# Kernel tuning notes

Measured on AMD Instinct MI355X. Metric: run time of the kernel, lower is better.

Reference implementation:

```python
import jax, jax.numpy as jnp
import numpy as np
from jax.scipy.special import logsumexp

E = 512      # input_size (= 2*hidden_size)
T = 24       # output_size (num CRF tags)
B, S = 32, 512
HEADS = 2


def setup_inputs() -> dict:
    key = jax.random.key(0)
    ks = jax.random.split(key, 12)
    u = lambda k, shape, a: jax.random.uniform(k, shape, jnp.float32, -a, a)
    inp = {
        "encoder_outputs": jax.random.normal(ks[0], (B, S, E), jnp.float32),
        "labels": jax.random.randint(ks[1], (B, S), 0, T),
        "mask": jnp.ones((B, S), dtype=bool),
        # nn.MultiheadAttention params
        "Win": u(ks[2], (3 * E, E), E ** -0.5),
        "bin_": jnp.zeros((3 * E,), jnp.float32),
        "Wout": u(ks[3], (E, E), E ** -0.5),
        "bout": jnp.zeros((E,), jnp.float32),
        # crf_linear
        "crf_w": u(ks[4], (T, E), E ** -0.5),
        "crf_b": u(ks[5], (T,), E ** -0.5),
        # torchcrf CRF params (uniform(-0.1, 0.1))
        "start_t": u(ks[6], (T,), 0.1),
        "end_t": u(ks[7], (T,), 0.1),
        "trans": u(ks[8], (T, T), 0.1),
        # entity_linear
        "ent_w": u(ks[9], (2, E), E ** -0.5),
        "ent_b": u(ks[10], (2,), E ** -0.5),
    }
    return inp


def _mha(x, Win, bin_, Wout, bout):
    b, s, e = x.shape
    hd = e // HEADS
    qkv = x @ Win.T + bin_                       # [B,S,3E]
    q, k, v = jnp.split(qkv, 3, axis=-1)
    q = q.reshape(b, s, HEADS, hd)
    k = k.reshape(b, s, HEADS, hd)
    v = v.reshape(b, s, HEADS, hd)
    scores = jnp.einsum("bqhd,bkhd->bhqk", q, k) / jnp.sqrt(jnp.float32(hd))
    attn = jax.nn.softmax(scores, axis=-1)       # [B,H,S,S]
    out = jnp.einsum("bhqk,bkhd->bqhd", attn, v).reshape(b, s, e)
    return out @ Wout.T + bout


def _crf_numerator(em, labels, maskf, start_t, end_t, trans):
    # em: [B,S,T] emissions, labels: [B,S] int, maskf: [B,S] float (mask[:,0]==1)
    bidx = jnp.arange(em.shape[0])
    score = start_t[labels[:, 0]] + em[bidx, 0, labels[:, 0]]
    prev, cur = labels[:, :-1], labels[:, 1:]
    em_t = jnp.take_along_axis(em[:, 1:], cur[:, :, None], axis=2)[..., 0]
    score = score + ((trans[prev, cur] + em_t) * maskf[:, 1:]).sum(axis=1)
    seq_ends = maskf.sum(axis=1).astype(jnp.int32) - 1
    last_tags = labels[bidx, seq_ends]
    return score + end_t[last_tags]


def _crf_normalizer(em, maskf, start_t, end_t, trans):
    score0 = start_t + em[:, 0]                  # [B,T]

    def step(score, x):
        e_t, m_t = x                             # [B,T], [B]
        nxt = logsumexp(score[:, :, None] + trans[None] + e_t[:, None, :], axis=1)
        return jnp.where(m_t[:, None] > 0, nxt, score), None

    xs = (em[:, 1:].swapaxes(0, 1), maskf[:, 1:].T)
    score, _ = jax.lax.scan(step, score0, xs)
    return logsumexp(score + end_t, axis=1)


def _viterbi(em, start_t, end_t, trans):
    # decode is called without a mask -> mask of all ones
    score0 = start_t + em[:, 0]                  # [B,T]

    def step(score, e_t):
        nxt = score[:, :, None] + trans[None] + e_t[:, None, :]  # [B,T,T]
        return nxt.max(axis=1), nxt.argmax(axis=1)

    score, history = jax.lax.scan(step, score0, em[:, 1:].swapaxes(0, 1))
    last = jnp.argmax(score + end_t, axis=1)     # [B]

    def back(tag, hist):
        prev = jnp.take_along_axis(hist, tag[:, None], axis=1)[:, 0]
        return prev, prev

    _, prevs = jax.lax.scan(back, last, history, reverse=True)  # [S-1,B]
    return jnp.concatenate([prevs, last[None]], axis=0).T       # [B,S]


def reference(encoder_outputs, labels, mask, Win, bin_, Wout, bout,
              crf_w, crf_b, start_t, end_t, trans, ent_w, ent_b):
    attn = _mha(encoder_outputs, Win, bin_, Wout, bout)
    dec = jax.nn.relu(attn)                      # [B,S,E]
    fc_out = dec @ crf_w.T + crf_b               # [B,S,T]
    maskf = mask.astype(fc_out.dtype)
    num = _crf_numerator(fc_out, labels, maskf, start_t, end_t, trans)
    den = _crf_normalizer(fc_out, maskf, start_t, end_t, trans)
    llh = (num - den).sum() / maskf.sum()        # reduction='token_mean'
    crf_out = _viterbi(fc_out, start_t, end_t, trans)
    seg_out = jax.nn.log_softmax(dec @ ent_w.T + ent_b, axis=2)
    return crf_out, seg_out, -llh
```

## Files before the change

### kernel.cpp

```cpp
#include <hip/hip_runtime.h>

#define BB 32
#define SS 512
#define EE 512
#define NHH 2
#define HDD 256
#define E3 1536
#define NT 24
#define MR (BB*SS)

typedef _Float16 half8  __attribute__((ext_vector_type(8)));
typedef _Float16 half4v __attribute__((ext_vector_type(4)));
typedef float    f32x4  __attribute__((ext_vector_type(4)));

__device__ __forceinline__ float rl(float v, int l) {
    return __int_as_float(__builtin_amdgcn_readlane(__float_as_int(v), l));
}

template<int BN>
__global__ __launch_bounds__(256) void mfma_gemm(
    const float* __restrict__ A, int lda, long sAhi, long sAlo, int zA,
    const float* __restrict__ B, int ldb, long sBhi, long sBlo, int zB,
    const float* __restrict__ bias,
    float* __restrict__ C, int ldc, long sChi, long sClo, int zC,
    int K, int relu)
{
    __shared__ __align__(16) _Float16 sAh[8*640];
    __shared__ __align__(16) _Float16 sAl[8*640];
    __shared__ __align__(16) _Float16 sBh[8*640];
    __shared__ __align__(16) _Float16 sBl[8*640];

    const int t = threadIdx.x;
    const int z = blockIdx.z;
    const int za = zA + z, zb = zB + z, zc = zC + z;
    const float* Ab = A + (size_t)(za>>1)*sAhi + (size_t)(za&1)*sAlo
                        + (size_t)blockIdx.y*128*lda;
    const float* Bb = B + (size_t)(zb>>1)*sBhi + (size_t)(zb&1)*sBlo
                        + (BN ? (size_t)blockIdx.x*128
                              : (size_t)blockIdx.x*128*ldb);

    const int wv = t >> 6, lane = t & 63;
    const int wm = wv >> 1, wn = wv & 1;
    const int lm = lane & 15, lq = lane >> 4;

    f32x4 acc[4][4];
#pragma unroll
    for (int i = 0; i < 4; ++i)
#pragma unroll
        for (int j = 0; j < 4; ++j) acc[i][j] = (f32x4){0.f,0.f,0.f,0.f};

    const int r8  = t >> 3;
    const int kc  = (t & 7) * 4;
    const int bnk = (t >> 7) * 16;
    const int bnn = t & 127;

    for (int k0 = 0; k0 < K; k0 += 32) {
        float4 ga[4], gb[4]; float gv[16];
#pragma unroll
        for (int i = 0; i < 4; ++i)
            ga[i] = *(const float4*)(Ab + (size_t)(r8 + 32*i)*lda + k0 + kc);
        if (BN) {
#pragma unroll
            for (int i = 0; i < 16; ++i)
                gv[i] = Bb[(size_t)(k0 + bnk + i)*ldb + bnn];
        } else {
#pragma unroll
            for (int i = 0; i < 4; ++i)
                gb[i] = *(const float4*)(Bb + (size_t)(r8 + 32*i)*ldb + k0 + kc);
        }
        __syncthreads();
#pragma unroll
        for (int i = 0; i < 4; ++i) {
            const int row  = r8 + 32*i;
            const int base = (row >> 4)*640 + (row & 15)*40 + kc;
            float4 a = ga[i];
            _Float16 h0 = (_Float16)a.x, h1 = (_Float16)a.y,
                     h2 = (_Float16)a.z, h3 = (_Float16)a.w;
            _Float16 l0 = (_Float16)(a.x - (float)h0),
                     l1 = (_Float16)(a.y - (float)h1),
                     l2 = (_Float16)(a.z - (float)h2),
                     l3 = (_Float16)(a.w - (float)h3);
            *(half4v*)&sAh[base] = (half4v){h0,h1,h2,h3};
            *(half4v*)&sAl[base] = (half4v){l0,l1,l2,l3};
        }
        if (BN) {
#pragma unroll
            for (int i = 0; i < 16; ++i) {
                const int k = bnk + i;
                float v = gv[i];
                _Float16 h = (_Float16)v;
                _Float16 l = (_Float16)(v - (float)h);
                const int base = (bnn >> 4)*640 + (bnn & 15)*40 + k;
                sBh[base] = h;
                sBl[base] = l;
            }
        } else {
#pragma unroll
            for (int i = 0; i < 4; ++i) {
                const int row  = r8 + 32*i;
                const int base = (row >> 4)*640 + (row & 15)*40 + kc;
                float4 b = gb[i];
                _Float16 h0 = (_Float16)b.x, h1 = (_Float16)b.y,
                         h2 = (_Float16)b.z, h3 = (_Float16)b.w;
                _Float16 l0 = (_Float16)(b.x - (float)h0),
                         l1 = (_Float16)(b.y - (float)h1),
                         l2 = (_Float16)(b.z - (float)h2),
                         l3 = (_Float16)(b.w - (float)h3);
                *(half4v*)&sBh[base] = (half4v){h0,h1,h2,h3};
                *(half4v*)&sBl[base] = (half4v){l0,l1,l2,l3};
            }
        }
        __syncthreads();

        half8 bhf[4], blf[4];
#pragma unroll
        for (int j = 0; j < 4; ++j) {
            const int tb = (wn*4 + j)*640 + lm*40 + lq*8;
            bhf[j] = *(const half8*)&sBh[tb];
            blf[j] = *(const half8*)&sBl[tb];
        }
#pragma unroll
        for (int i = 0; i < 4; ++i) {
            const int ta = (wm*4 + i)*640 + lm*40 + lq*8;
            half8 ah = *(const half8*)&sAh[ta];
            half8 al = *(const half8*)&sAl[ta];
#pragma unroll
            for (int j = 0; j < 4; ++j) {
                acc[i][j] = __builtin_amdgcn_mfma_f32_16x16x32_f16(ah, bhf[j], acc[i][j], 0, 0, 0);
                acc[i][j] = __builtin_amdgcn_mfma_f32_16x16x32_f16(al, bhf[j], acc[i][j], 0, 0, 0);
                acc[i][j] = __builtin_amdgcn_mfma_f32_16x16x32_f16(ah, blf[j], acc[i][j], 0, 0, 0);
            }
        }
    }

    float* Cb = C + (size_t)(zc>>1)*sChi + (size_t)(zc&1)*sClo;
#pragma unroll
    for (int j = 0; j < 4; ++j) {
        const int col = blockIdx.x*128 + (wn*4 + j)*16 + lm;
        const float bj = bias ? bias[col] : 0.f;
#pragma unroll
        for (int i = 0; i < 4; ++i) {
            const int row0 = blockIdx.y*128 + (wm*4 + i)*16 + lq*4;
#pragma unroll
            for (int r = 0; r < 4; ++r) {
                float v = acc[i][j][r] + bj;
                if (relu) v = fmaxf(v, 0.f);
                Cb[(size_t)(row0 + r)*ldc + col] = v;
            }
        }
    }
}

__global__ __launch_bounds__(256) void softmax_rows(float* __restrict__ scores)
{
    const int w    = threadIdx.x >> 6;
    const int lane = threadIdx.x & 63;
    const size_t row = (size_t)blockIdx.x * 4 + w;
    float* p = scores + row * SS + lane * 8;
    float4 v0 = *(float4*)(p);
    float4 v1 = *(float4*)(p + 4);
    const float scale = 0.0625f;
    float m = fmaxf(fmaxf(fmaxf(v0.x, v0.y), fmaxf(v0.z, v0.w)),
                    fmaxf(fmaxf(v1.x, v1.y), fmaxf(v1.z, v1.w)));
#pragma unroll
    for (int off = 32; off >= 1; off >>= 1) m = fmaxf(m, __shfl_xor(m, off));
    v0.x = __expf((v0.x - m) * scale); v0.y = __expf((v0.y - m) * scale);
    v0.z = __expf((v0.z - m) * scale); v0.w = __expf((v0.w - m) * scale);
    v1.x = __expf((v1.x - m) * scale); v1.y = __expf((v1.y - m) * scale);
    v1.z = __expf((v1.z - m) * scale); v1.w = __expf((v1.w - m) * scale);
    float sum = v0.x + v0.y + v0.z + v0.w + v1.x + v1.y + v1.z + v1.w;
#pragma unroll
    for (int off = 32; off >= 1; off >>= 1) sum += __shfl_xor(sum, off);
    float inv = 1.f / sum;
    v0.x *= inv; v0.y *= inv; v0.z *= inv; v0.w *= inv;
    v1.x *= inv; v1.y *= inv; v1.z *= inv; v1.w *= inv;
    *(float4*)(p)     = v0;
    *(float4*)(p + 4) = v1;
}

__global__ __launch_bounds__(192) void fc_crf_kernel(
    const float* __restrict__ dec, const float* __restrict__ W,
    const float* __restrict__ bias, float* __restrict__ out)
{
    __shared__ __align__(16) float Ws[NT][516];
    for (int i = threadIdx.x; i < NT*128; i += 192) {
        int j = i >> 7, c = (i & 127) * 4;
        *(float4*)&Ws[j][c] = *(const float4*)(W + (size_t)j*EE + c);
    }
    __syncthreads();
    const int t = threadIdx.x;
    const int rloc = t / NT;
    const int j = t - rloc * NT;
    const int row = blockIdx.x * 8 + rloc;
    const float4* a = (const float4*)(dec + (size_t)row * EE);
    float acc = 0.f;
#pragma unroll 4
    for (int i = 0; i < 128; ++i) {
        float4 x = a[i];
        float4 y = *(const float4*)&Ws[j][i*4];
        acc += x.x*y.x + x.y*y.y + x.z*y.z + x.w*y.w;
    }
    out[(size_t)row * NT + j] = acc + bias[j];
}

__global__ __launch_bounds__(64, 1) void crf_seg_kernel(
    const float* __restrict__ fc, const int* __restrict__ labels,
    const float* __restrict__ start_t, const float* __restrict__ end_t,
    const float* __restrict__ trans, const float* __restrict__ dec,
    const float* __restrict__ ent_w, const float* __restrict__ ent_b,
    float* __restrict__ num, float* __restrict__ den,
    float* __restrict__ crf_out, float* __restrict__ segout)
{
    __shared__ __align__(16) float fc_lds[SS*NT];
    __shared__ unsigned char hist[(SS-1)*NT];

    const int blk  = blockIdx.x;
    const int lane = threadIdx.x;

    if (blk >= 96) {
        const int row = blk - 96;
        const float4* a  = (const float4*)(dec + (size_t)row * EE);
        const float4* w0 = (const float4*)(ent_w);
        const float4* w1 = (const float4*)(ent_w + EE);
        float acc0 = 0.f, acc1 = 0.f;
#pragma unroll
        for (int i = 0; i < 2; ++i) {
            int idx = lane * 2 + i;
            float4 x = a[idx];
            float4 u = w0[idx];
            float4 v = w1[idx];
            acc0 += x.x*u.x + x.y*u.y + x.z*u.z + x.w*u.w;
            acc1 += x.x*v.x + x.y*v.y + x.z*v.z + x.w*v.w;
        }
#pragma unroll
        for (int off = 32; off >= 1; off >>= 1) {
            acc0 += __shfl_xor(acc0, off);
            acc1 += __shfl_xor(acc1, off);
        }
        if (lane == 0) {
            float l0 = acc0 + ent_b[0];
            float l1 = acc1 + ent_b[1];
            float m  = fmaxf(l0, l1);
            float lse = m + __logf(__expf(l0 - m) + __expf(l1 - m));
            segout[(size_t)row*2 + 0] = l0 - lse;
            segout[(size_t)row*2 + 1] = l1 - lse;
        }
        return;
    }

    const int role = blk >> 5;
    const int b    = blk & 31;
    const float* fcb = fc + (size_t)b * SS * NT;

    if (role == 2) {
        float acc = 0.f;
        for (int s = 1 + lane; s < SS; s += 64) {
            int prev = labels[b*SS + s - 1];
            int cur  = labels[b*SS + s];
            acc += trans[prev*NT + cur] + fcb[(size_t)s*NT + cur];
        }
        if (lane == 0) {
            int l0 = labels[b*SS];
            acc += start_t[l0] + fcb[l0] + end_t[labels[b*SS + SS - 1]];
        }
#pragma unroll
        for (int off = 32; off >= 1; off >>= 1) acc += __shfl_xor(acc, off);
        if (lane == 0) num[b] = acc;
        return;
    }

#pragma unroll
    for (int i = 0; i < SS*NT/256; ++i) {
        const int idx = i*256 + lane*4;
        *(float4*)&fc_lds[idx] = *(const float4*)(fcb + idx);
    }
    __syncthreads();

    const int j = (lane < NT) ? lane : 0;
    float sc = start_t[j] + fc_lds[j];

    if (role == 0) {
        float etr[NT];
#pragma unroll
        for (int i = 0; i < NT; ++i) etr[i] = __expf(trans[i*NT + j]);
        float em_next = fc_lds[NT + j];
        for (int s = 1; s < SS; ++s) {
            float em = em_next;
            int snx = (s + 1 < SS) ? s + 1 : s;
            em_next = fc_lds[snx * NT + j];
            const float m  = __builtin_amdgcn_readfirstlane(sc);
            const float eo = __expf(sc - m);
            float a0 = 0.f, a1 = 0.f, a2 = 0.f, a3 = 0.f;
#pragma unroll
            for (int i = 0; i < NT; i += 4) {
                a0 = fmaf(rl(eo, i+0), etr[i+0], a0);
                a1 = fmaf(rl(eo, i+1), etr[i+1], a1);
                a2 = fmaf(rl(eo, i+2), etr[i+2], a2);
                a3 = fmaf(rl(eo, i+3), etr[i+3], a3);
            }
            sc = m + __logf((a0 + a1) + (a2 + a3)) + em;
        }
        float v = (lane < NT) ? sc + end_t[j] : -1e30f;
        float m2 = v;
#pragma unroll
        for (int off = 32; off >= 1; off >>= 1) m2 = fmaxf(m2, __shfl_xor(m2, off));
        float e = (lane < NT) ? __expf(v - m2) : 0.f;
#pragma unroll
        for (int off = 32; off >= 1; off >>= 1) e += __shfl_xor(e, off);
        if (lane == 0) den[b] = m2 + __logf(e);
    } else {
        float trC[NT];
#pragma unroll
        for (int i = 0; i < NT; ++i) trC[i] = trans[i*NT + j];
        float em_next = fc_lds[NT + j];
        for (int s = 1; s < SS; ++s) {
            float em = em_next;
            int snx = (s + 1 < SS) ? s + 1 : s;
            em_next = fc_lds[snx * NT + j];
            float tv[NT]; int ti[NT];
#pragma unroll
            for (int i = 0; i < NT; ++i) { tv[i] = rl(sc, i) + trC[i]; ti[i] = i; }
#pragma unroll
            for (int st = 1; st < NT; st <<= 1)
#pragma unroll
                for (int i = 0; i + st < NT; i += 2*st)
                    if (tv[i+st] > tv[i]) { tv[i] = tv[i+st]; ti[i] = ti[i+st]; }
            sc = tv[0] + em;
            if (lane < NT) hist[(s-1)*NT + lane] = (unsigned char)ti[0];
        }
        float bv = (lane < NT) ? sc + end_t[j] : -1e30f;
        int bi = (lane < NT) ? lane : NT;
#pragma unroll
        for (int off = 32; off >= 1; off >>= 1) {
            float ov = __shfl_xor(bv, off);
            int   oi = __shfl_xor(bi, off);
            if (ov > bv || (ov == bv && oi < bi)) { bv = ov; bi = oi; }
        }
        __syncthreads();
        if (lane == 0) {
            int tag = bi;
            crf_out[(size_t)b*SS + SS - 1] = (float)tag;
            for (int s = SS - 2; s >= 0; --s) {
                tag = hist[s*NT + tag];
                crf_out[(size_t)b*SS + s] = (float)tag;
            }
        }
    }
}

__global__ __launch_bounds__(64) void llh_kernel(
    const float* __restrict__ num, const float* __restrict__ den,
    float* __restrict__ out)
{
    int t = threadIdx.x;
    float v = (t < BB) ? (num[t] - den[t]) : 0.f;
#pragma unroll
    for (int off = 32; off >= 1; off >>= 1) v += __shfl_xor(v, off);
    if (t == 0) out[(size_t)MR * 3] = -(v / (float)MR);
}

extern "C" void kernel_launch(void* const* d_in, const int* in_sizes, int n_in,
                              void* d_out, int out_size, void* d_ws, size_t ws_size,
                              hipStream_t stream) {
    const float* enc     = (const float*)d_in[0];
    const int*   labels  = (const int*)  d_in[1];
    const float* Win     = (const float*)d_in[3];
    const float* bin     = (const float*)d_in[4];
    const float* Wout    = (const float*)d_in[5];
    const float* bout    = (const float*)d_in[6];
    const float* crf_w   = (const float*)d_in[7];
    const float* crf_b   = (const float*)d_in[8];
    const float* start_t = (const float*)d_in[9];
    const float* end_t   = (const float*)d_in[10];
    const float* trans   = (const float*)d_in[11];
    const float* ent_w   = (const float*)d_in[12];
    const float* ent_b   = (const float*)d_in[13];
    float* out = (float*)d_out;

    float* ws   = (float*)d_ws;
    float* qkv  = ws;
    float* attn = qkv  + (size_t)MR * E3;
    float* big  = attn + (size_t)MR * EE;
    float* sch  = big;
    float* dec  = big;
    float* fc   = big  + (size_t)MR * EE;
    float* num  = fc   + (size_t)MR * NT;
    float* den  = num  + BB;

    dim3 blk(256);
    mfma_gemm<0><<<dim3(E3/128, MR/128, 1), blk, 0, stream>>>(
        enc, EE, 0, 0, 0,  Win, EE, 0, 0, 0,  bin,
        qkv, E3, 0, 0, 0,  EE, 0);
    for (int p = 0; p < 2; ++p) {
        int zoff = p * 32;
        mfma_gemm<0><<<dim3(SS/128, SS/128, 32), blk, 0, stream>>>(
            qkv,      E3, (long)SS*E3, HDD, zoff,
            qkv + EE, E3, (long)SS*E3, HDD, zoff,
            nullptr,
            sch, SS, 2L*SS*SS, (long)SS*SS, 0,
            HDD, 0);
        softmax_rows<<<(32*SS)/4, blk, 0, stream>>>(sch);
        mfma_gemm<1><<<dim3(HDD/128, SS/128, 32), blk, 0, stream>>>(
            sch, SS, 2L*SS*SS, (long)SS*SS, 0,
            qkv + 2*EE, E3, (long)SS*E3, HDD, zoff,
            nullptr,
            attn, EE, (long)SS*EE, HDD, zoff,
            SS, 0);
    }
    mfma_gemm<0><<<dim3(EE/128, MR/128, 1), blk, 0, stream>>>(
        attn, EE, 0, 0, 0,  Wout, EE, 0, 0, 0,  bout,
        dec, EE, 0, 0, 0,  EE, 1);
    fc_crf_kernel<<<MR/8, dim3(192), 0, stream>>>(dec, crf_w, crf_b, fc);
    crf_seg_kernel<<<96 + MR, dim3(64), 0, stream>>>(
        fc, labels, start_t, end_t, trans, dec, ent_w, ent_b,
        num, den, out, out + MR);
    llh_kernel<<<1, 64, 0, stream>>>(num, den, out);
}
```

Measured before the change: 563.9 us.

## Store GEMM intermediates pre-split as packed fp16 hi/lo pairs

The fp32-to-fp16 hi/lo split is moved out of each GEMM's shared-memory staging. Producers (the QKV GEMM epilogue, the softmax, and a new pre-pass over encoder outputs) now write packed 32-bit hi/lo words, and consumers unpack them with byte permutes. This removes repeated conversion work and reorganises the V-operand load into vectorised row loads instead of strided scalar loads. The cost is an extra split_pack pass over the input and byte-granular scatter stores into LDS for the V operand.

```diff
diff --git a/kernel.cpp b/kernel.cpp
--- a/kernel.cpp
+++ b/kernel.cpp
@@ -12,17 +12,45 @@
 typedef _Float16 half8  __attribute__((ext_vector_type(8)));
 typedef _Float16 half4v __attribute__((ext_vector_type(4)));
 typedef float    f32x4  __attribute__((ext_vector_type(4)));
+typedef unsigned int u32;
 
 __device__ __forceinline__ float rl(float v, int l) {
     return __int_as_float(__builtin_amdgcn_readlane(__float_as_int(v), l));
 }
 
-template<int BN>
-__global__ __launch_bounds__(256) void mfma_gemm(
-    const float* __restrict__ A, int lda, long sAhi, long sAlo, int zA,
-    const float* __restrict__ B, int ldb, long sBhi, long sBlo, int zB,
+__device__ __forceinline__ u32 packhl(float v) {
+    _Float16 h = (_Float16)v;
+    _Float16 l = (_Float16)(v - (float)h);
+    unsigned short hb, lb;
+    __builtin_memcpy(&hb, &h, 2);
+    __builtin_memcpy(&lb, &l, 2);
+    return (u32)hb | ((u32)lb << 16);
+}
+__device__ __forceinline__ _Float16 hl_lo(u32 u) {
+    unsigned short s = (unsigned short)(u & 0xFFFFu);
+    _Float16 f; __builtin_memcpy(&f, &s, 2); return f;
+}
+__device__ __forceinline__ _Float16 hl_hi(u32 u) {
+    unsigned short s = (unsigned short)(u >> 16);
+    _Float16 f; __builtin_memcpy(&f, &s, 2); return f;
+}
+
+__global__ __launch_bounds__(256) void split_pack(
+    const float* __restrict__ in, u32* __restrict__ out)
+{
+    const size_t i = ((size_t)blockIdx.x * 256 + threadIdx.x) * 4;
+    float4 v = *(const float4*)(in + i);
+    uint4 o;
+    o.x = packhl(v.x); o.y = packhl(v.y); o.z = packhl(v.z); o.w = packhl(v.w);
+    *(uint4*)(out + i) = o;
+}
+
+template<int BFMT, int EPACK>
+__global__ __launch_bounds__(256) void mfma_gemm_p(
+    const u32* __restrict__ Ap, int lda, long sAhi, long sAlo, int zA,
+    const void* __restrict__ Bp, int ldb, long sBhi, long sBlo, int zB,
     const float* __restrict__ bias,
-    float* __restrict__ C, int ldc, long sChi, long sClo, int zC,
+    void* __restrict__ C, int ldc, long sChi, long sClo, int zC,
     int K, int relu)
 {
     __shared__ __align__(16) _Float16 sAh[8*640];
@@ -33,11 +61,13 @@
     const int t = threadIdx.x;
     const int z = blockIdx.z;
     const int za = zA + z, zb = zB + z, zc = zC + z;
-    const float* Ab = A + (size_t)(za>>1)*sAhi + (size_t)(za&1)*sAlo
-                        + (size_t)blockIdx.y*128*lda;
-    const float* Bb = B + (size_t)(zb>>1)*sBhi + (size_t)(zb&1)*sBlo
-                        + (BN ? (size_t)blockIdx.x*128
-                              : (size_t)blockIdx.x*128*ldb);
+    const u32* Ab = Ap + (size_t)(za>>1)*sAhi + (size_t)(za&1)*sAlo
+                       + (size_t)blockIdx.y*128*lda;
+    const size_t boff = (size_t)(zb>>1)*sBhi + (size_t)(zb&1)*sBlo
+                      + (BFMT == 2 ? (size_t)blockIdx.x*128
+                                   : (size_t)blockIdx.x*128*ldb);
+    const float* Bf = (const float*)Bp + boff;
+    const u32*   Bu = (const u32*)Bp + boff;
 
     const int wv = t >> 6, lane = t & 63;
     const int wm = wv >> 1, wn = wv & 1;
@@ -49,57 +79,51 @@
 #pragma unroll
         for (int j = 0; j < 4; ++j) acc[i][j] = (f32x4){0.f,0.f,0.f,0.f};
 
-    const int r8  = t >> 3;
-    const int kc  = (t & 7) * 4;
-    const int bnk = (t >> 7) * 16;
-    const int bnn = t & 127;
+    const int r8 = t >> 3;
+    const int kc = (t & 7) * 4;
+    const int vk  = t >> 3;
+    const int vns = (t & 7) * 16;
 
     for (int k0 = 0; k0 < K; k0 += 32) {
-        float4 ga[4], gb[4]; float gv[16];
+        uint4 ga[4]; float4 gbf[4]; uint4 gbu[4]; u32 vv[16];
 #pragma unroll
         for (int i = 0; i < 4; ++i)
-            ga[i] = *(const float4*)(Ab + (size_t)(r8 + 32*i)*lda + k0 + kc);
-        if (BN) {
-#pragma unroll
-            for (int i = 0; i < 16; ++i)
-                gv[i] = Bb[(size_t)(k0 + bnk + i)*ldb + bnn];
+            ga[i] = *(const uint4*)(Ab + (size_t)(r8 + 32*i)*lda + k0 + kc);
+        if (BFMT == 0) {
+#pragma unroll
+            for (int i = 0; i < 4; ++i)
+                gbf[i] = *(const float4*)(Bf + (size_t)(r8 + 32*i)*ldb + k0 + kc);
+        } else if (BFMT == 1) {
+#pragma unroll
+            for (int i = 0; i < 4; ++i)
+                gbu[i] = *(const uint4*)(Bu + (size_t)(r8 + 32*i)*ldb + k0 + kc);
         } else {
 #pragma unroll
-            for (int i = 0; i < 4; ++i)
-                gb[i] = *(const float4*)(Bb + (size_t)(r8 + 32*i)*ldb + k0 + kc);
+            for (int jj = 0; jj < 4; ++jj) {
+                uint4 u = *(const uint4*)(Bu + (size_t)(k0 + vk)*ldb + vns + jj*4);
+                vv[jj*4+0]=u.x; vv[jj*4+1]=u.y; vv[jj*4+2]=u.z; vv[jj*4+3]=u.w;
+            }
         }
         __syncthreads();
 #pragma unroll
         for (int i = 0; i < 4; ++i) {
             const int row  = r8 + 32*i;
             const int base = (row >> 4)*640 + (row & 15)*40 + kc;
-            float4 a = ga[i];
-            _Float16 h0 = (_Float16)a.x, h1 = (_Float16)a.y,
-                     h2 = (_Float16)a.z, h3 = (_Float16)a.w;
-            _Float16 l0 = (_Float16)(a.x - (float)h0),
-                     l1 = (_Float16)(a.y - (float)h1),
-                     l2 = (_Float16)(a.z - (float)h2),
-                     l3 = (_Float16)(a.w - (float)h3);
-            *(half4v*)&sAh[base] = (half4v){h0,h1,h2,h3};
-            *(half4v*)&sAl[base] = (half4v){l0,l1,l2,l3};
-        }
-        if (BN) {
-#pragma unroll
-            for (int i = 0; i < 16; ++i) {
-                const int k = bnk + i;
-                float v = gv[i];
-                _Float16 h = (_Float16)v;
-                _Float16 l = (_Float16)(v - (float)h);
-                const int base = (bnn >> 4)*640 + (bnn & 15)*40 + k;
-                sBh[base] = h;
-                sBl[base] = l;
-            }
-        } else {
+            uint4 u = ga[i];
+            uint2 hs, ls;
+            hs.x = __builtin_amdgcn_perm(u.y, u.x, 0x05040100u);
+            hs.y = __builtin_amdgcn_perm(u.w, u.z, 0x05040100u);
+            ls.x = __builtin_amdgcn_perm(u.y, u.x, 0x07060302u);
+            ls.y = __builtin_amdgcn_perm(u.w, u.z, 0x07060302u);
+            *(uint2*)&sAh[base] = hs;
+            *(uint2*)&sAl[base] = ls;
+        }
+        if (BFMT == 0) {
 #pragma unroll
             for (int i = 0; i < 4; ++i) {
                 const int row  = r8 + 32*i;
                 const int base = (row >> 4)*640 + (row & 15)*40 + kc;
-                float4 b = gb[i];
+                float4 b = gbf[i];
                 _Float16 h0 = (_Float16)b.x, h1 = (_Float16)b.y,
                          h2 = (_Float16)b.z, h3 = (_Float16)b.w;
                 _Float16 l0 = (_Float16)(b.x - (float)h0),
@@ -109,6 +133,28 @@
                 *(half4v*)&sBh[base] = (half4v){h0,h1,h2,h3};
                 *(half4v*)&sBl[base] = (half4v){l0,l1,l2,l3};
             }
+        } else if (BFMT == 1) {
+#pragma unroll
+            for (int i = 0; i < 4; ++i) {
+                const int row  = r8 + 32*i;
+                const int base = (row >> 4)*640 + (row & 15)*40 + kc;
+                uint4 u = gbu[i];
+                uint2 hs, ls;
+                hs.x = __builtin_amdgcn_perm(u.y, u.x, 0x05040100u);
+                hs.y = __builtin_amdgcn_perm(u.w, u.z, 0x05040100u);
+                ls.x = __builtin_amdgcn_perm(u.y, u.x, 0x07060302u);
+                ls.y = __builtin_amdgcn_perm(u.w, u.z, 0x07060302u);
+                *(uint2*)&sBh[base] = hs;
+                *(uint2*)&sBl[base] = ls;
+            }
+        } else {
+            const int vt = (vns >> 4) * 640;
+#pragma unroll
+            for (int e = 0; e < 16; ++e) {
+                const int base = vt + ((vns + e) & 15)*40 + vk;
+                sBh[base] = hl_lo(vv[e]);
+                sBl[base] = hl_hi(vv[e]);
+            }
         }
         __syncthreads();
 
@@ -133,7 +179,9 @@
         }
     }
 
-    float* Cb = C + (size_t)(zc>>1)*sChi + (size_t)(zc&1)*sClo;
+    const size_t coff = (size_t)(zc>>1)*sChi + (size_t)(zc&1)*sClo;
+    float* Cf = (float*)C + coff;
+    u32*   Cu = (u32*)C + coff;
 #pragma unroll
     for (int j = 0; j < 4; ++j) {
         const int col = blockIdx.x*128 + (wn*4 + j)*16 + lm;
@@ -145,13 +193,14 @@
             for (int r = 0; r < 4; ++r) {
                 float v = acc[i][j][r] + bj;
                 if (relu) v = fmaxf(v, 0.f);
-                Cb[(size_t)(row0 + r)*ldc + col] = v;
-            }
-        }
-    }
-}
-
-__global__ __launch_bounds__(256) void softmax_rows(float* __restrict__ scores)
+                if (EPACK) Cu[(size_t)(row0 + r)*ldc + col] = packhl(v);
+                else       Cf[(size_t)(row0 + r)*ldc + col] = v;
+            }
+        }
+    }
+}
+
+__global__ __launch_bounds__(256) void softmax_split(float* __restrict__ scores)
 {
     const int w    = threadIdx.x >> 6;
     const int lane = threadIdx.x & 63;
@@ -172,10 +221,14 @@
 #pragma unroll
     for (int off = 32; off >= 1; off >>= 1) sum += __shfl_xor(sum, off);
     float inv = 1.f / sum;
-    v0.x *= inv; v0.y *= inv; v0.z *= inv; v0.w *= inv;
-    v1.x *= inv; v1.y *= inv; v1.z *= inv; v1.w *= inv;
-    *(float4*)(p)     = v0;
-    *(float4*)(p + 4) = v1;
+    uint4 o0, o1;
+    o0.x = packhl(v0.x*inv); o0.y = packhl(v0.y*inv);
+    o0.z = packhl(v0.z*inv); o0.w = packhl(v0.w*inv);
+    o1.x = packhl(v1.x*inv); o1.y = packhl(v1.y*inv);
+    o1.z = packhl(v1.z*inv); o1.w = packhl(v1.w*inv);
+    u32* up = (u32*)(scores + row * SS) + lane * 8;
+    *(uint4*)(up)     = o0;
+    *(uint4*)(up + 4) = o1;
 }
 
 __global__ __launch_bounds__(192) void fc_crf_kernel(
@@ -377,38 +430,39 @@
     const float* ent_b   = (const float*)d_in[13];
     float* out = (float*)d_out;
 
-    float* ws   = (float*)d_ws;
-    float* qkv  = ws;
-    float* attn = qkv  + (size_t)MR * E3;
-    float* big  = attn + (size_t)MR * EE;
+    u32*   qkvp = (u32*)d_ws;
+    u32*   encp = qkvp + (size_t)MR * E3;
+    u32*   attnp = encp;
+    float* big  = (float*)(encp + (size_t)MR * EE);
     float* sch  = big;
     float* dec  = big;
-    float* fc   = big  + (size_t)MR * EE;
-    float* num  = fc   + (size_t)MR * NT;
-    float* den  = num  + BB;
+    float* fc   = big + (size_t)MR * EE;
+    float* num  = fc  + (size_t)MR * NT;
+    float* den  = num + BB;
 
     dim3 blk(256);
-    mfma_gemm<0><<<dim3(E3/128, MR/128, 1), blk, 0, stream>>>(
-        enc, EE, 0, 0, 0,  Win, EE, 0, 0, 0,  bin,
-        qkv, E3, 0, 0, 0,  EE, 0);
+    split_pack<<<(MR*EE)/1024, blk, 0, stream>>>(enc, encp);
+    mfma_gemm_p<0,1><<<dim3(E3/128, MR/128, 1), blk, 0, stream>>>(
+        encp, EE, 0, 0, 0,  Win, EE, 0, 0, 0,  bin,
+        qkvp, E3, 0, 0, 0,  EE, 0);
     for (int p = 0; p < 2; ++p) {
         int zoff = p * 32;
-        mfma_gemm<0><<<dim3(SS/128, SS/128, 32), blk, 0, stream>>>(
-            qkv,      E3, (long)SS*E3, HDD, zoff,
-            qkv + EE, E3, (long)SS*E3, HDD, zoff,
+        mfma_gemm_p<1,0><<<dim3(SS/128, SS/128, 32), blk, 0, stream>>>(
+            qkvp,      E3, (long)SS*E3, HDD, zoff,
+            qkvp + EE, E3, (long)SS*E3, HDD, zoff,
             nullptr,
             sch, SS, 2L*SS*SS, (long)SS*SS, 0,
             HDD, 0);
-        softmax_rows<<<(32*SS)/4, blk, 0, stream>>>(sch);
-        mfma_gemm<1><<<dim3(HDD/128, SS/128, 32), blk, 0, stream>>>(
-            sch, SS, 2L*SS*SS, (long)SS*SS, 0,
-            qkv + 2*EE, E3, (long)SS*E3, HDD, zoff,
+        softmax_split<<<(32*SS)/4, blk, 0, stream>>>(sch);
+        mfma_gemm_p<2,1><<<dim3(HDD/128, SS/128, 32), blk, 0, stream>>>(
+            (u32*)sch, SS, 2L*SS*SS, (long)SS*SS, 0,
+            qkvp + 2*EE, E3, (long)SS*E3, HDD, zoff,
             nullptr,
-            attn, EE, (long)SS*EE, HDD, zoff,
+            attnp, EE, (long)SS*EE, HDD, zoff,
             SS, 0);
     }
-    mfma_gemm<0><<<dim3(EE/128, MR/128, 1), blk, 0, stream>>>(
-        attn, EE, 0, 0, 0,  Wout, EE, 0, 0, 0,  bout,
+    mfma_gemm_p<0,0><<<dim3(EE/128, MR/128, 1), blk, 0, stream>>>(
+        attnp, EE, 0, 0, 0,  Wout, EE, 0, 0, 0,  bout,
         dec, EE, 0, 0, 0,  EE, 1);
     fc_crf_kernel<<<MR/8, dim3(192), 0, stream>>>(dec, crf_w, crf_b, fc);
     crf_seg_kernel<<<96 + MR, dim3(64), 0, stream>>>(
```

Result: slower. 597.1 us (+5.9%).
